# Kernel tuning notes

Measured on AMD Instinct MI355X. Metric: run time of the kernel, lower is better.

Reference implementation:

```python
import jax, jax.numpy as jnp
import numpy as np

B, N, C, H = 4, 2048, 1024, 16
HD = C // H  # head_dim = 64


def setup_inputs() -> dict:
    key = jax.random.key(0)
    ks = jax.random.split(key, 16)
    s = 0.02
    return {
        "x": jax.random.normal(ks[0], (B, N, C), dtype=jnp.float32),
        # qkv_proj: Linear(C, 3C): weight (3C, C), bias (3C,)
        "W_qkv": jax.random.normal(ks[1], (3 * C, C), dtype=jnp.float32) * s,
        "b_qkv": jax.random.normal(ks[2], (3 * C,), dtype=jnp.float32) * s,
        # out_proj: Linear(C, C)
        "W_out": jax.random.normal(ks[3], (C, C), dtype=jnp.float32) * s,
        "b_out": jax.random.normal(ks[4], (C,), dtype=jnp.float32) * s,
        # dynamically-reassigned position bias: shape (1, N, H, H) per the code's
        # (B, num_heads=N, seq_len=H, seq_len=H) score tensor
        "pos_bias": jax.random.normal(ks[5], (1, N, H, H), dtype=jnp.float32) * 0.01,
        # conv_proj: Linear(C, C)
        "W_cp": jax.random.normal(ks[6], (C, C), dtype=jnp.float32) * s,
        "b_cp": jax.random.normal(ks[7], (C,), dtype=jnp.float32) * s,
        # pointwise Conv1d(C, C, k=1): weight (C, C) after squeezing kernel dim
        "W_pw": jax.random.normal(ks[8], (C, C), dtype=jnp.float32) * s,
        "b_pw": jax.random.normal(ks[9], (C,), dtype=jnp.float32) * s,
        # depthwise Conv1d(C, C, k=3, groups=C): weight (C, 3)
        "W_dw": jax.random.normal(ks[10], (C, 3), dtype=jnp.float32) * s,
        "b_dw": jax.random.normal(ks[11], (C,), dtype=jnp.float32) * s,
        # token_wise_proj: Linear(C, C)
        "W_tw": jax.random.normal(ks[12], (C, C), dtype=jnp.float32) * s,
        "b_tw": jax.random.normal(ks[13], (C,), dtype=jnp.float32) * s,
    }


def reference(x, W_qkv, b_qkv, W_out, b_out, pos_bias, W_cp, b_cp,
              W_pw, b_pw, W_dw, b_dw, W_tw, b_tw) -> jnp.ndarray:
    Bx, Nx, Cx = x.shape
    scale = HD ** -0.5
    # qkv -> (B, N, H, 3*HD), chunk into q,k,v of (B, N, H, HD).
    # NOTE: faithful to the torch code, heads stay on axis 2; the matmul
    # contracts head_dim giving (B, N, H, H) scores (attention over heads).
    qkv = (x @ W_qkv.T + b_qkv).reshape(Bx, Nx, H, 3 * HD)
    q, k, v = jnp.split(qkv, 3, axis=-1)
    scores = jnp.einsum('bnhd,bngd->bnhg', q, k) * scale + pos_bias
    attn = jax.nn.softmax(scores, axis=-1)
    attn_out = jnp.einsum('bnhg,bngd->bnhd', attn, v).reshape(Bx, Nx, Cx)
    attn_out = attn_out @ W_out.T + b_out

    # Convolutional branch
    xc = x @ W_cp.T + b_cp          # conv_proj
    xc = xc @ W_pw.T + b_pw          # pointwise conv (k=1) == linear over channels
    xp = jnp.pad(xc, ((0, 0), (1, 1), (0, 0)))  # pad seq for k=3, padding=1
    xc = (xp[:, :-2] * W_dw[:, 0] + xp[:, 1:-1] * W_dw[:, 1]
          + xp[:, 2:] * W_dw[:, 2] + b_dw)      # depthwise conv
    xc = xc @ W_tw.T + b_tw          # token_wise_proj

    return attn_out + xc
```

## Files before the change

kernel.cpp:

```cpp
#include <hip/hip_runtime.h>
#include <hip/hip_bf16.h>
#include <stdint.h>

typedef __bf16 bf16_t;
typedef __attribute__((ext_vector_type(8))) __bf16 bf16x8;
typedef __attribute__((ext_vector_type(4))) __bf16 bf16x4;
typedef __attribute__((ext_vector_type(4))) float floatx4;
typedef __attribute__((ext_vector_type(4))) _Float16 half4_t;

#define GLDS16(g, l)                                                          \
  __builtin_amdgcn_global_load_lds(                                           \
      (const __attribute__((address_space(1))) void*)(g),                     \
      (__attribute__((address_space(3))) void*)(l), 16, 0, 0)

#define BAR8                                                                  \
  do {                                                                        \
    __builtin_amdgcn_s_barrier();                                             \
    __builtin_amdgcn_sched_barrier(0);                                        \
  } while (0)
#define VMCNT(n) asm volatile("s_waitcnt vmcnt(" #n ")")

template <int IT, int JT, typename OT>
__global__ __launch_bounds__(256) void gemm_bt(
    const bf16_t* __restrict__ A, const bf16_t* __restrict__ B,
    const float* __restrict__ bias, OT* __restrict__ C, int M, int N, int K) {
  constexpr int AROWS = 32 * IT;
  constexpr int BROWS = 32 * JT;
  constexpr int COLS = BROWS;
  constexpr int STAGE = (AROWS + BROWS) * 64;
  constexpr int EPI = (sizeof(OT) == 2) ? AROWS * COLS : 0;
  constexpr int SME = STAGE > EPI ? STAGE : EPI;
  __shared__ bf16_t sm[SME];
  bf16_t* As = sm;
  bf16_t* Bs = sm + AROWS * 64;

  const int tid = threadIdx.x;
  const int wave = tid >> 6;
  const int lane = tid & 63;
  const int quad = lane >> 4;
  const int l16 = lane & 15;
  const int m0 = blockIdx.x * AROWS;
  const int n0 = blockIdx.y * BROWS;
  const int wm = (wave >> 1) * (IT * 16);
  const int wn = (wave & 1) * (JT * 16);

  const int ra = wave * (8 * IT) + (lane >> 3);
  const int ga = ((lane & 7) ^ (ra & 7)) * 8;
  const int rb = wave * (8 * JT) + (lane >> 3);
  const int gb = ((lane & 7) ^ (rb & 7)) * 8;
  const bf16_t* Ab = A + (size_t)(m0 + ra) * K + ga;
  const bf16_t* Bb = B + (size_t)(n0 + rb) * K + gb;
  const int p0 = (quad ^ (l16 & 7)) * 8;

  floatx4 acc[IT][JT];
  const floatx4 zf = {0.f, 0.f, 0.f, 0.f};
#pragma unroll
  for (int i = 0; i < IT; ++i)
#pragma unroll
    for (int j = 0; j < JT; ++j) acc[i][j] = zf;

  for (int k0 = 0; k0 < K; k0 += 64) {
#pragma unroll
    for (int t = 0; t < IT; ++t)
      GLDS16(Ab + (size_t)(t * 8) * K + k0, As + (wave * (64 * IT) + t * 64) * 8);
#pragma unroll
    for (int t = 0; t < JT; ++t)
      GLDS16(Bb + (size_t)(t * 8) * K + k0, Bs + (wave * (64 * JT) + t * 64) * 8);
    __syncthreads();
#pragma unroll
    for (int ks = 0; ks < 2; ++ks) {
      const int ko = p0 ^ (ks * 32);
      bf16x8 af[IT], bfr[JT];
#pragma unroll
      for (int i = 0; i < IT; ++i)
        af[i] = *(const bf16x8*)(As + (wm + i * 16 + l16) * 64 + ko);
#pragma unroll
      for (int j = 0; j < JT; ++j)
        bfr[j] = *(const bf16x8*)(Bs + (wn + j * 16 + l16) * 64 + ko);
#pragma unroll
      for (int i = 0; i < IT; ++i)
#pragma unroll
        for (int j = 0; j < JT; ++j)
          acc[i][j] = __builtin_amdgcn_mfma_f32_16x16x32_bf16(
              bfr[j], af[i], acc[i][j], 0, 0, 0);
    }
    __syncthreads();
  }

  if constexpr (sizeof(OT) == 4) {
#pragma unroll
    for (int j = 0; j < JT; ++j) {
      const int colb = n0 + wn + j * 16 + quad * 4;
      floatx4 bv = zf;
      if (bias) bv = *(const floatx4*)(bias + colb);
#pragma unroll
      for (int i = 0; i < IT; ++i) {
        const int row = m0 + wm + i * 16 + l16;
        floatx4 v = acc[i][j] + bv;
        *(floatx4*)((float*)C + (size_t)row * N + colb) = v;
      }
    }
  } else {
    constexpr int SWZ = COLS / 32;
    constexpr int CPR = COLS / 8;
    constexpr int PASSES = (AROWS * CPR) / 256;
#pragma unroll
    for (int j = 0; j < JT; ++j) {
      const int colb = n0 + wn + j * 16 + quad * 4;
      floatx4 bv = zf;
      if (bias) bv = *(const floatx4*)(bias + colb);
      const int gcol = (wn + j * 16 + quad * 4) >> 2;
#pragma unroll
      for (int i = 0; i < IT; ++i) {
        const int rl = wm + i * 16 + l16;
        floatx4 v = acc[i][j] + bv;
        union {
          bf16_t b[4];
          uint2 u2;
        } pk;
        pk.b[0] = (bf16_t)v[0];
        pk.b[1] = (bf16_t)v[1];
        pk.b[2] = (bf16_t)v[2];
        pk.b[3] = (bf16_t)v[3];
        const int gsw = gcol ^ ((rl & 7) * SWZ);
        *(uint2*)(sm + rl * COLS + gsw * 4) = pk.u2;
      }
    }
    __syncthreads();
    bf16_t* Cb = (bf16_t*)C;
#pragma unroll
    for (int pass = 0; pass < PASSES; ++pass) {
      const int f = pass * 256 + tid;
      const int row = f / CPR;
      const int c16 = f % CPR;
      const int g0 = (2 * c16) ^ ((row & 7) * SWZ);
      uint4 v = *(const uint4*)(sm + row * COLS + g0 * 4);
      *(uint4*)(Cb + (size_t)(m0 + row) * N + n0 + c16 * 8) = v;
    }
  }
}

__global__ __launch_bounds__(512, 2) void gemm8p(
    const bf16_t* __restrict__ A, const bf16_t* __restrict__ B,
    const float* __restrict__ bias, bf16_t* __restrict__ C, int M, int N,
    int K) {
  __shared__ bf16_t sm8[65536];
  bf16_t* As = sm8;
  bf16_t* Bs = sm8 + 32768;

  const int tid = threadIdx.x;
  const int wave = tid >> 6, lane = tid & 63;
  const int l16 = lane & 15, quad = lane >> 4;
  const int wm = (wave >> 2) * 128, wn = (wave & 3) * 64;

  const int lin = blockIdx.y * gridDim.x + blockIdx.x;
  const int nwg = gridDim.x * gridDim.y;
  const int chunk = nwg >> 3;
  const int swz = (lin & 7) * chunk + (lin >> 3);
  const int bm = swz / gridDim.x;
  const int bn = swz % gridDim.x;
  const int m0 = bm << 8, n0 = bn << 8;

  const int srow = wave * 32 + (lane >> 2);
  const int kswz = ((lane & 3) * 8) ^ ((lane >> 5) << 4);
  const bf16_t* Ag = A + (size_t)(m0 + srow) * K + kswz;
  const bf16_t* Bg = B + (size_t)(n0 + srow) * K + kswz;
  const int sdst = wave * 1024;
  const size_t a16k = (size_t)K << 4;

  const int koe = (quad * 8) ^ ((l16 & 8) << 1);
  const int aoff = (wm + l16) * 32 + koe;
  const int boff = (wn + l16) * 32 + koe;

  floatx4 acc[8][4];
  const floatx4 zf = {0.f, 0.f, 0.f, 0.f};
#pragma unroll
  for (int i = 0; i < 8; ++i)
#pragma unroll
    for (int j = 0; j < 4; ++j) acc[i][j] = zf;

  bf16x8 af[4], bfr[4];

#define STG_A(buf, kh, TOFF)                                     \
  do {                                                           \
    bf16_t* _d = As + (buf)*16384 + (kh)*8192 + sdst;            \
    GLDS16(Ag + (TOFF) + (kh)*32, _d);                           \
    GLDS16(Ag + a16k + (TOFF) + (kh)*32, _d + 512);              \
  } while (0)
#define STG_B(buf, kh, TOFF)                                     \
  do {                                                           \
    bf16_t* _d = Bs + (buf)*16384 + (kh)*8192 + sdst;            \
    GLDS16(Bg + (TOFF) + (kh)*32, _d);                           \
    GLDS16(Bg + a16k + (TOFF) + (kh)*32, _d + 512);              \
  } while (0)
#define LDA4(buf, ks, mb)                                        \
  do {                                                           \
    const bf16_t* _p = As + (buf)*16384 + (ks)*8192 + aoff + (mb)*512; \
    af[0] = *(const bf16x8*)(_p);                                \
    af[1] = *(const bf16x8*)(_p + 512);                          \
    af[2] = *(const bf16x8*)(_p + 1024);                         \
    af[3] = *(const bf16x8*)(_p + 1536);                         \
  } while (0)
#define LDB4(buf, ks)                                            \
  do {                                                           \
    const bf16_t* _p = Bs + (buf)*16384 + (ks)*8192 + boff;      \
    bfr[0] = *(const bf16x8*)(_p);                               \
    bfr[1] = *(const bf16x8*)(_p + 512);                         \
    bfr[2] = *(const bf16x8*)(_p + 1024);                        \
    bfr[3] = *(const bf16x8*)(_p + 1536);                        \
  } while (0)
#define MFMA16(mb)                                               \
  do {                                                           \
    __builtin_amdgcn_s_setprio(1);                               \
    _Pragma("unroll") for (int _i = 0; _i < 4; ++_i)             \
        _Pragma("unroll") for (int _j = 0; _j < 4; ++_j)         \
            acc[(mb) + _i][_j] =                                 \
                __builtin_amdgcn_mfma_f32_16x16x32_bf16(         \
                    bfr[_j], af[_i], acc[(mb) + _i][_j], 0, 0, 0); \
    __builtin_amdgcn_s_setprio(0);                               \
  } while (0)

  STG_A(0, 0, 0);
  STG_A(0, 1, 0);
  STG_B(0, 0, 0);
  STG_B(0, 1, 0);
  STG_B(1, 0, 64);
  STG_A(1, 0, 64);
  STG_B(1, 1, 64);
  VMCNT(6);
  BAR8;

  const int NT = K >> 6;
  for (int it = 0; it < NT / 2 - 1; ++it) {
    LDA4(0, 0, 0); LDB4(0, 0); STG_A(1, 1, 64);            BAR8; MFMA16(0); BAR8;
    LDA4(0, 0, 4);             STG_B(0, 0, 128);           BAR8; MFMA16(4); BAR8;
    LDA4(0, 1, 0); LDB4(0, 1); STG_A(0, 0, 128);           BAR8; MFMA16(0); BAR8;
    LDA4(0, 1, 4);             STG_B(0, 1, 128); VMCNT(6); BAR8; MFMA16(4); BAR8;
    LDA4(1, 0, 0); LDB4(1, 0); STG_A(0, 1, 128);           BAR8; MFMA16(0); BAR8;
    LDA4(1, 0, 4);             STG_B(1, 0, 192);           BAR8; MFMA16(4); BAR8;
    LDA4(1, 1, 0); LDB4(1, 1); STG_A(1, 0, 192);           BAR8; MFMA16(0); BAR8;
    LDA4(1, 1, 4);             STG_B(1, 1, 192); VMCNT(6); BAR8; MFMA16(4); BAR8;
    Ag += 128;
    Bg += 128;
  }
  LDA4(0, 0, 0); LDB4(0, 0); STG_A(1, 1, 64); BAR8; MFMA16(0); BAR8;
  LDA4(0, 0, 4);                              BAR8; MFMA16(4); BAR8;
  LDA4(0, 1, 0); LDB4(0, 1);                  BAR8; MFMA16(0); BAR8;
  LDA4(0, 1, 4);             VMCNT(0);        BAR8; MFMA16(4); BAR8;
  LDA4(1, 0, 0); LDB4(1, 0);                  BAR8; MFMA16(0); BAR8;
  LDA4(1, 0, 4);                              BAR8; MFMA16(4); BAR8;
  LDA4(1, 1, 0); LDB4(1, 1);                  BAR8; MFMA16(0); BAR8;
  LDA4(1, 1, 4);                              BAR8; MFMA16(4); BAR8;

  const int crow_b = wm + l16;
#pragma unroll
  for (int nj = 0; nj < 4; ++nj) {
    const int colb = wn + nj * 16 + quad * 4;
    floatx4 bv = zf;
    if (bias) bv = *(const floatx4*)(bias + n0 + colb);
#pragma unroll
    for (int mi = 0; mi < 8; ++mi) {
      const int row = crow_b + mi * 16;
      floatx4 v = acc[mi][nj] + bv;
      union {
        bf16_t b[4];
        uint2 u2;
      } pk;
      pk.b[0] = (bf16_t)v[0];
      pk.b[1] = (bf16_t)v[1];
      pk.b[2] = (bf16_t)v[2];
      pk.b[3] = (bf16_t)v[3];
      const int cb = (colb * 2) ^ ((row & 31) << 4);
      *(uint2*)((char*)sm8 + row * 512 + cb) = pk.u2;
    }
  }
  __syncthreads();
#pragma unroll
  for (int pass = 0; pass < 16; ++pass) {
    const int flat = pass * 8192 + tid * 16;
    const int row = flat >> 9;
    const int cb = flat & 511;
    const int cbs = cb ^ ((row & 31) << 4);
    uint4 v = *(const uint4*)((char*)sm8 + row * 512 + cbs);
    *(uint4*)((char*)C + ((size_t)(m0 + row) * N + n0) * 2 + cb) = v;
  }
#undef STG_A
#undef STG_B
#undef LDA4
#undef LDB4
#undef MFMA16
}

__global__ __launch_bounds__(512, 2) void gemm8p2(
    const bf16_t* __restrict__ A, const bf16_t* __restrict__ B,
    const float* __restrict__ bias, float* __restrict__ C, int M, int N,
    int K) {
  __shared__ bf16_t sm2[49152];
  bf16_t* As = sm2;
  bf16_t* Bs = sm2 + 16384;

  const int tid = threadIdx.x;
  const int wave = tid >> 6, lane = tid & 63;
  const int l16 = lane & 15, quad = lane >> 4;
  const int wm = (wave >> 2) * 64, wn = (wave & 3) * 64;
  const int m0 = blockIdx.y << 7, n0 = blockIdx.x << 8;

  const int srA = wave * 16 + (lane >> 2);
  const int srB = wave * 32 + (lane >> 2);
  const int kswz = ((lane & 3) * 8) ^ ((lane >> 5) << 4);
  const bf16_t* Ag = A + (size_t)(m0 + srA) * K + kswz;
  const bf16_t* Bg = B + (size_t)(n0 + srB) * K + kswz;
  const size_t b16k = (size_t)K << 4;

  const int koe = (quad * 8) ^ ((l16 & 8) << 1);
  const int aoff = (wm + l16) * 32 + koe;
  const int boff = (wn + l16) * 32 + koe;

  floatx4 acc[4][4];
  const floatx4 zf = {0.f, 0.f, 0.f, 0.f};
#pragma unroll
  for (int i = 0; i < 4; ++i)
#pragma unroll
    for (int j = 0; j < 4; ++j) acc[i][j] = zf;

  bf16x8 af[4], bfr[4];

#define SA2(buf, kh, TOFF)                                                 \
  GLDS16(Ag + (TOFF) + (kh)*32, As + (buf)*8192 + (kh)*4096 + wave * 512)
#define SB2(buf, kh, TOFF)                                                 \
  do {                                                                     \
    bf16_t* _d = Bs + (buf)*16384 + (kh)*8192 + wave * 1024;               \
    GLDS16(Bg + (TOFF) + (kh)*32, _d);                                     \
    GLDS16(Bg + b16k + (TOFF) + (kh)*32, _d + 512);                        \
  } while (0)
#define LD2(buf, kh)                                                       \
  do {                                                                     \
    const bf16_t* _pa = As + (buf)*8192 + (kh)*4096 + aoff;                \
    const bf16_t* _pb = Bs + (buf)*16384 + (kh)*8192 + boff;               \
    _Pragma("unroll") for (int _i = 0; _i < 4; ++_i)                       \
        af[_i] = *(const bf16x8*)(_pa + _i * 512);                         \
    _Pragma("unroll") for (int _j = 0; _j < 4; ++_j)                       \
        bfr[_j] = *(const bf16x8*)(_pb + _j * 512);                        \
  } while (0)
#define MM2                                                                \
  do {                                                                     \
    __builtin_amdgcn_s_setprio(1);                                         \
    _Pragma("unroll") for (int _i = 0; _i < 4; ++_i)                       \
        _Pragma("unroll") for (int _j = 0; _j < 4; ++_j)                   \
            acc[_i][_j] = __builtin_amdgcn_mfma_f32_16x16x32_bf16(         \
                bfr[_j], af[_i], acc[_i][_j], 0, 0, 0);                    \
    __builtin_amdgcn_s_setprio(0);                                         \
  } while (0)

  SA2(0, 0, 0);
  SB2(0, 0, 0);
  SA2(0, 1, 0);
  SB2(0, 1, 0);
  SA2(1, 0, 64);
  SB2(1, 0, 64);
  VMCNT(3);
  BAR8;

  const int NT = K >> 6;
  for (int it = 0; it < NT / 2 - 1; ++it) {
    LD2(0, 0); SA2(1, 1, 64);  SB2(1, 1, 64);            BAR8; MM2; BAR8;
    LD2(0, 1); SA2(0, 0, 128); SB2(0, 0, 128); VMCNT(3); BAR8; MM2; BAR8;
    LD2(1, 0); SA2(0, 1, 128); SB2(0, 1, 128);           BAR8; MM2; BAR8;
    LD2(1, 1); SA2(1, 0, 192); SB2(1, 0, 192); VMCNT(3); BAR8; MM2; BAR8;
    Ag += 128;
    Bg += 128;
  }
  LD2(0, 0); SA2(1, 1, 64); SB2(1, 1, 64); BAR8; MM2; BAR8;
  LD2(0, 1); VMCNT(0);                     BAR8; MM2; BAR8;
  LD2(1, 0);                               BAR8; MM2; BAR8;
  LD2(1, 1);                                     MM2;

#pragma unroll
  for (int j = 0; j < 4; ++j) {
    const int colb = n0 + wn + j * 16 + quad * 4;
    floatx4 bv = zf;
    if (bias) bv = *(const floatx4*)(bias + colb);
#pragma unroll
    for (int i = 0; i < 4; ++i) {
      const int row = m0 + wm + i * 16 + l16;
      floatx4 v = acc[i][j] + bv;
      *(floatx4*)(C + (size_t)row * N + colb) = v;
    }
  }
#undef SA2
#undef SB2
#undef LD2
#undef MM2
}

__global__ __launch_bounds__(256) void prep2_k(
    const float* __restrict__ x, bf16_t* __restrict__ x_bf,
    const float* __restrict__ Wqkv, bf16_t* __restrict__ Wbig1,
    const float* __restrict__ Wpw, bf16_t* __restrict__ Wpw_bf,
    const float* __restrict__ Wout, const float* __restrict__ Wtw,
    bf16_t* __restrict__ Wbig2, const float* __restrict__ bqkv,
    float* __restrict__ bias1, const float* __restrict__ bout,
    const float* __restrict__ btw, float* __restrict__ bias2,
    const float* __restrict__ Wcp, bf16_t* __restrict__ WcpT,
    const float* __restrict__ bcp, const float* __restrict__ bpw) {
  __shared__ float t[32][33];
  const int b = blockIdx.x, tid = threadIdx.x;
  auto cvt4 = [](const float* in, bf16_t* out, int i) {
    floatx4 v = ((const floatx4*)in)[i];
    bf16x4 o;
    o[0] = (bf16_t)v[0];
    o[1] = (bf16_t)v[1];
    o[2] = (bf16_t)v[2];
    o[3] = (bf16_t)v[3];
    ((bf16x4*)out)[i] = o;
  };
  if (b < 8192) {
    cvt4(x, x_bf, b * 256 + tid);
  } else if (b < 11264) {
    cvt4(Wqkv, Wbig1, (b - 8192) * 256 + tid);
  } else if (b < 12288) {
    cvt4(Wpw, Wpw_bf, (b - 11264) * 256 + tid);
  } else if (b < 14336) {
    const bool second = b >= 13312;
    int i = (b - (second ? 13312 : 12288)) * 256 + tid;
    floatx4 v = ((const floatx4*)(second ? Wtw : Wout))[i];
    bf16x4 o;
    o[0] = (bf16_t)v[0];
    o[1] = (bf16_t)v[1];
    o[2] = (bf16_t)v[2];
    o[3] = (bf16_t)v[3];
    int row = i >> 8, c4 = i & 255;
    *(bf16x4*)(Wbig2 + (size_t)row * 2048 + (second ? 1024 : 0) + c4 * 4) = o;
  } else if (b < 14339) {
    int i = (b - 14336) * 256 + tid;
    if (i < 768) ((floatx4*)bias1)[i] = ((const floatx4*)bqkv)[i];
  } else if (b == 14339) {
    ((floatx4*)bias2)[tid] =
        ((const floatx4*)bout)[tid] + ((const floatx4*)btw)[tid];
  } else if (b < 15364) {
    const int tb = b - 14340;
    const int bx = (tb & 31) * 32, by = (tb >> 5) * 32;
    const int tx = tid & 31, ty = tid >> 5;
#pragma unroll
    for (int iq = 0; iq < 4; ++iq)
      t[ty + iq * 8][tx] = Wcp[(size_t)(by + ty + iq * 8) * 1024 + bx + tx];
    __syncthreads();
#pragma unroll
    for (int iq = 0; iq < 4; ++iq)
      WcpT[(size_t)(bx + ty + iq * 8) * 1024 + by + tx] =
          (bf16_t)t[tx][ty + iq * 8];
  } else {
    const int row = (b - 15364) * 4 + (tid >> 6);
    const int l = tid & 63;
    const float* wr = Wpw + (size_t)row * 1024;
    float s = 0.f;
    for (int j = l; j < 1024; j += 64) s += wr[j] * bcp[j];
#pragma unroll
    for (int o = 32; o > 0; o >>= 1) s += __shfl_down(s, o);
    if (l == 0) bias1[3072 + row] = s + bpw[row];
  }
}

static __device__ inline void exp8(uint32_t w0, uint32_t w1, uint32_t w2,
                                   uint32_t w3, float* f) {
  f[0] = __uint_as_float(w0 << 16);
  f[1] = __uint_as_float(w0 & 0xffff0000u);
  f[2] = __uint_as_float(w1 << 16);
  f[3] = __uint_as_float(w1 & 0xffff0000u);
  f[4] = __uint_as_float(w2 << 16);
  f[5] = __uint_as_float(w2 & 0xffff0000u);
  f[6] = __uint_as_float(w3 << 16);
  f[7] = __uint_as_float(w3 & 0xffff0000u);
}

__global__ __launch_bounds__(256) void mid_k(const bf16_t* __restrict__ G1,
                                             const float* __restrict__ pos,
                                             const float* __restrict__ Wdw,
                                             const float* __restrict__ bdw,
                                             bf16_t* __restrict__ Mid) {
  __shared__ bf16_t ost[4][16 * 68];
  const int tid = threadIdx.x;
  if (blockIdx.x < 2048) {
    const int wave = tid >> 6, lane = tid & 63;
    const int p = blockIdx.x * 4 + wave;
    const int l16 = lane & 15, quad = lane >> 4;
    const bf16_t* row = G1 + (size_t)p * 4096;
    const bf16_t* qb = row + l16 * 192 + quad * 8;

    bf16x8 q0 = *(const bf16x8*)(qb);
    bf16x8 q1 = *(const bf16x8*)(qb + 32);
    bf16x8 k0 = *(const bf16x8*)(qb + 64);
    bf16x8 k1 = *(const bf16x8*)(qb + 96);
    floatx4 S = {0.f, 0.f, 0.f, 0.f};
    S = __builtin_amdgcn_mfma_f32_16x16x32_bf16(k0, q0, S, 0, 0, 0);
    S = __builtin_amdgcn_mfma_f32_16x16x32_bf16(k1, q1, S, 0, 0, 0);

    const floatx4 pb = *(const floatx4*)(pos + (size_t)(p & 2047) * 256 +
                                         l16 * 16 + quad * 4);
    float v[4];
#pragma unroll
    for (int r = 0; r < 4; ++r) v[r] = S[r] * 0.125f + pb[r];

    float m = fmaxf(fmaxf(v[0], v[1]), fmaxf(v[2], v[3]));
    m = fmaxf(m, __shfl_xor(m, 16));
    m = fmaxf(m, __shfl_xor(m, 32));
    float e[4], sum = 0.f;
#pragma unroll
    for (int r = 0; r < 4; ++r) {
      e[r] = __expf(v[r] - m);
      sum += e[r];
    }
    sum += __shfl_xor(sum, 16);
    sum += __shfl_xor(sum, 32);
    const float inv = 1.0f / sum;
    half4_t pa;
#pragma unroll
    for (int r = 0; r < 4; ++r) pa[r] = (_Float16)(e[r] * inv);

    const bf16_t* vb_base = row + 128 + l16;
    const floatx4 zf = {0.f, 0.f, 0.f, 0.f};
    floatx4 o[4];
#pragma unroll
    for (int t = 0; t < 4; ++t) {
      half4_t vb;
#pragma unroll
      for (int j = 0; j < 4; ++j)
        vb[j] = (_Float16)(float)vb_base[(quad * 4 + j) * 192 + t * 16];
      o[t] = __builtin_amdgcn_mfma_f32_16x16x16f16(pa, vb, zf, 0, 0, 0);
    }

    bf16_t* ow = ost[wave];
#pragma unroll
    for (int r = 0; r < 4; ++r)
#pragma unroll
      for (int t = 0; t < 4; ++t)
        ow[(quad * 4 + r) * 68 + t * 16 + l16] = (bf16_t)o[t][r];
    const int h2 = lane >> 2, m4 = lane & 3;
    const bf16_t* srcp = ow + h2 * 68 + m4 * 16;
    uint2 a0 = *(const uint2*)(srcp);
    uint2 a1 = *(const uint2*)(srcp + 4);
    uint2 a2 = *(const uint2*)(srcp + 8);
    uint2 a3 = *(const uint2*)(srcp + 12);
    uint4 s0 = {a0.x, a0.y, a1.x, a1.y};
    uint4 s1 = {a2.x, a2.y, a3.x, a3.y};
    uint4* dst = (uint4*)(Mid + (size_t)p * 2048 + h2 * 64 + m4 * 16);
    dst[0] = s0;
    dst[1] = s1;
  } else {
    const bf16_t* in = G1 + 3072;
    bf16_t* out = Mid + 1024;
    const int item = (blockIdx.x - 2048) * 256 + tid;
    const int cc = item & 127, rowg = item >> 7;
    const int c0 = cc * 8;
    float w0[8], w1[8], w2[8], bb[8];
#pragma unroll
    for (int c = 0; c < 8; ++c) {
      w0[c] = Wdw[(c0 + c) * 3];
      w1[c] = Wdw[(c0 + c) * 3 + 1];
      w2[c] = Wdw[(c0 + c) * 3 + 2];
      bb[c] = bdw[c0 + c];
    }
#pragma unroll
    for (int jr = 0; jr < 4; ++jr) {
      const int tt = rowg * 4 + jr;
      const int n = tt & 2047;
      const bf16_t* ip = in + (size_t)tt * 4096 + c0;
      const uint4 z4 = {0, 0, 0, 0};
      uint4 um = (n > 0) ? *(const uint4*)(ip - 4096) : z4;
      uint4 uc = *(const uint4*)(ip);
      uint4 up = (n < 2047) ? *(const uint4*)(ip + 4096) : z4;
      float fm[8], fc[8], fp[8];
      exp8(um.x, um.y, um.z, um.w, fm);
      exp8(uc.x, uc.y, uc.z, uc.w, fc);
      exp8(up.x, up.y, up.z, up.w, fp);
      union {
        bf16_t b[8];
        uint4 u;
      } pk;
#pragma unroll
      for (int c = 0; c < 8; ++c)
        pk.b[c] =
            (bf16_t)(bb[c] + fm[c] * w0[c] + fc[c] * w1[c] + fp[c] * w2[c]);
      *(uint4*)(out + (size_t)tt * 2048 + c0) = pk.u;
    }
  }
}

extern "C" void kernel_launch(void* const* d_in, const int* in_sizes, int n_in,
                              void* d_out, int out_size, void* d_ws,
                              size_t ws_size, hipStream_t stream) {
  (void)in_sizes; (void)n_in; (void)out_size; (void)ws_size;
  const float* x = (const float*)d_in[0];
  const float* Wqkv = (const float*)d_in[1];
  const float* bqkv = (const float*)d_in[2];
  const float* Wout = (const float*)d_in[3];
  const float* bout = (const float*)d_in[4];
  const float* pos = (const float*)d_in[5];
  const float* Wcp = (const float*)d_in[6];
  const float* bcp = (const float*)d_in[7];
  const float* Wpw = (const float*)d_in[8];
  const float* bpw = (const float*)d_in[9];
  const float* Wdw = (const float*)d_in[10];
  const float* bdw = (const float*)d_in[11];
  const float* Wtw = (const float*)d_in[12];
  const float* btw = (const float*)d_in[13];
  float* out = (float*)d_out;

  char* ws = (char*)d_ws;
  const size_t MB = 1024ull * 1024ull;
  bf16_t* x_bf = (bf16_t*)(ws + 0);
  bf16_t* Wbig1 = (bf16_t*)(ws + 16 * MB);
  bf16_t* WcpT = (bf16_t*)(ws + 24 * MB);
  bf16_t* Wpw_bf = (bf16_t*)(ws + 26 * MB);
  bf16_t* Mid = (bf16_t*)(ws + 0);
  bf16_t* Wbig2 = (bf16_t*)(ws + 32 * MB);
  float* bias1 = (float*)(ws + 36 * MB);
  float* bias2 = (float*)(ws + 36 * MB + 65536);
  bf16_t* G1out = (bf16_t*)(ws + 37 * MB);

  prep2_k<<<15620, 256, 0, stream>>>(x, x_bf, Wqkv, Wbig1, Wpw, Wpw_bf, Wout,
                                     Wtw, Wbig2, bqkv, bias1, bout, btw, bias2,
                                     Wcp, WcpT, bcp, bpw);

  gemm_bt<2, 2, bf16_t><<<dim3(16, 16), 256, 0, stream>>>(
      Wpw_bf, WcpT, nullptr, Wbig1 + (size_t)3072 * 1024, 1024, 1024, 1024);

  gemm8p<<<dim3(16, 32), 512, 0, stream>>>(x_bf, Wbig1, bias1, G1out, 8192,
                                           4096, 1024);

  mid_k<<<3072, 256, 0, stream>>>(G1out, pos, Wdw, bdw, Mid);

  gemm8p2<<<dim3(4, 64), 512, 0, stream>>>(Mid, Wbig2, bias2, out, 8192, 1024,
                                           2048);
}
```

Before: 275.7 us.

## Double-buffer LDS fragment registers to prefetch next MFMA operands early

Both GEMM kernels now keep two sets of A/B fragment registers and load the next sub-tile from LDS one stage ahead of the MFMA block that consumes the current set, so LDS read latency overlaps matrix math. The global-to-LDS staging waits (vmcnt) are reshuffled to match the new ordering, the MFMA loop order is swapped to iterate j outermost, and an explicit sync is added before the epilogue. The extra fragment registers raise VGPR pressure, which may hurt occupancy, and the retuned wait counts must still guarantee LDS data is ready before it is read.

```diff
diff --git a/kernel.cpp b/kernel.cpp
--- a/kernel.cpp
+++ b/kernel.cpp
@@ -179,7 +179,7 @@
 #pragma unroll
     for (int j = 0; j < 4; ++j) acc[i][j] = zf;
 
-  bf16x8 af[4], bfr[4];
+  bf16x8 afA[4], afB[4], bfr[4];
 
 #define STG_A(buf, kh, TOFF)                                     \
   do {                                                           \
@@ -192,14 +192,6 @@
     bf16_t* _d = Bs + (buf)*16384 + (kh)*8192 + sdst;            \
     GLDS16(Bg + (TOFF) + (kh)*32, _d);                           \
     GLDS16(Bg + a16k + (TOFF) + (kh)*32, _d + 512);              \
-  } while (0)
-#define LDA4(buf, ks, mb)                                        \
-  do {                                                           \
-    const bf16_t* _p = As + (buf)*16384 + (ks)*8192 + aoff + (mb)*512; \
-    af[0] = *(const bf16x8*)(_p);                                \
-    af[1] = *(const bf16x8*)(_p + 512);                          \
-    af[2] = *(const bf16x8*)(_p + 1024);                         \
-    af[3] = *(const bf16x8*)(_p + 1536);                         \
   } while (0)
 #define LDB4(buf, ks)                                            \
   do {                                                           \
@@ -209,14 +201,23 @@
     bfr[2] = *(const bf16x8*)(_p + 1024);                        \
     bfr[3] = *(const bf16x8*)(_p + 1536);                        \
   } while (0)
-#define MFMA16(mb)                                               \
+#define LDA4(buf, ks, mb, DST)                                   \
+  do {                                                           \
+    const bf16_t* _p =                                           \
+        As + (buf)*16384 + (ks)*8192 + aoff + (mb)*512;          \
+    DST[0] = *(const bf16x8*)(_p);                               \
+    DST[1] = *(const bf16x8*)(_p + 512);                         \
+    DST[2] = *(const bf16x8*)(_p + 1024);                        \
+    DST[3] = *(const bf16x8*)(_p + 1536);                        \
+  } while (0)
+#define MFMA16(AF, mb)                                           \
   do {                                                           \
     __builtin_amdgcn_s_setprio(1);                               \
-    _Pragma("unroll") for (int _i = 0; _i < 4; ++_i)             \
-        _Pragma("unroll") for (int _j = 0; _j < 4; ++_j)         \
+    _Pragma("unroll") for (int _j = 0; _j < 4; ++_j)             \
+        _Pragma("unroll") for (int _i = 0; _i < 4; ++_i)         \
             acc[(mb) + _i][_j] =                                 \
                 __builtin_amdgcn_mfma_f32_16x16x32_bf16(         \
-                    bfr[_j], af[_i], acc[(mb) + _i][_j], 0, 0, 0); \
+                    bfr[_j], AF[_i], acc[(mb) + _i][_j], 0, 0, 0); \
     __builtin_amdgcn_s_setprio(0);                               \
   } while (0)
 
@@ -229,28 +230,30 @@
   STG_B(1, 1, 64);
   VMCNT(6);
   BAR8;
+  LDA4(0, 0, 0, afA);
 
   const int NT = K >> 6;
   for (int it = 0; it < NT / 2 - 1; ++it) {
-    LDA4(0, 0, 0); LDB4(0, 0); STG_A(1, 1, 64);            BAR8; MFMA16(0); BAR8;
-    LDA4(0, 0, 4);             STG_B(0, 0, 128);           BAR8; MFMA16(4); BAR8;
-    LDA4(0, 1, 0); LDB4(0, 1); STG_A(0, 0, 128);           BAR8; MFMA16(0); BAR8;
-    LDA4(0, 1, 4);             STG_B(0, 1, 128); VMCNT(6); BAR8; MFMA16(4); BAR8;
-    LDA4(1, 0, 0); LDB4(1, 0); STG_A(0, 1, 128);           BAR8; MFMA16(0); BAR8;
-    LDA4(1, 0, 4);             STG_B(1, 0, 192);           BAR8; MFMA16(4); BAR8;
-    LDA4(1, 1, 0); LDB4(1, 1); STG_A(1, 0, 192);           BAR8; MFMA16(0); BAR8;
-    LDA4(1, 1, 4);             STG_B(1, 1, 192); VMCNT(6); BAR8; MFMA16(4); BAR8;
+    LDB4(0, 0); LDA4(0, 0, 4, afB); STG_A(1, 1, 64);  VMCNT(8); BAR8; MFMA16(afA, 0); BAR8;
+    LDA4(0, 1, 0, afA);             STG_B(0, 0, 128);           BAR8; MFMA16(afB, 4); BAR8;
+    LDB4(0, 1); LDA4(0, 1, 4, afB); STG_A(0, 0, 128); VMCNT(8); BAR8; MFMA16(afA, 0); BAR8;
+    LDA4(1, 0, 0, afA);             STG_B(0, 1, 128);           BAR8; MFMA16(afB, 4); BAR8;
+    LDB4(1, 0); LDA4(1, 0, 4, afB); STG_A(0, 1, 128); VMCNT(8); BAR8; MFMA16(afA, 0); BAR8;
+    LDA4(1, 1, 0, afA);             STG_B(1, 0, 192);           BAR8; MFMA16(afB, 4); BAR8;
+    LDB4(1, 1); LDA4(1, 1, 4, afB); STG_A(1, 0, 192); VMCNT(8); BAR8; MFMA16(afA, 0); BAR8;
+    LDA4(0, 0, 0, afA);             STG_B(1, 1, 192);           BAR8; MFMA16(afB, 4); BAR8;
     Ag += 128;
     Bg += 128;
   }
-  LDA4(0, 0, 0); LDB4(0, 0); STG_A(1, 1, 64); BAR8; MFMA16(0); BAR8;
-  LDA4(0, 0, 4);                              BAR8; MFMA16(4); BAR8;
-  LDA4(0, 1, 0); LDB4(0, 1);                  BAR8; MFMA16(0); BAR8;
-  LDA4(0, 1, 4);             VMCNT(0);        BAR8; MFMA16(4); BAR8;
-  LDA4(1, 0, 0); LDB4(1, 0);                  BAR8; MFMA16(0); BAR8;
-  LDA4(1, 0, 4);                              BAR8; MFMA16(4); BAR8;
-  LDA4(1, 1, 0); LDB4(1, 1);                  BAR8; MFMA16(0); BAR8;
-  LDA4(1, 1, 4);                              BAR8; MFMA16(4); BAR8;
+  LDB4(0, 0); LDA4(0, 0, 4, afB); STG_A(1, 1, 64); VMCNT(8); BAR8; MFMA16(afA, 0); BAR8;
+  LDA4(0, 1, 0, afA);                                         BAR8; MFMA16(afB, 4); BAR8;
+  LDB4(0, 1); LDA4(0, 1, 4, afB);                  VMCNT(4); BAR8; MFMA16(afA, 0); BAR8;
+  LDA4(1, 0, 0, afA);                                         BAR8; MFMA16(afB, 4); BAR8;
+  LDB4(1, 0); LDA4(1, 0, 4, afB);                  VMCNT(0); BAR8; MFMA16(afA, 0); BAR8;
+  LDA4(1, 1, 0, afA);                                         BAR8; MFMA16(afB, 4); BAR8;
+  LDB4(1, 1); LDA4(1, 1, 4, afB);                             BAR8; MFMA16(afA, 0); BAR8;
+  MFMA16(afB, 4);
+  __syncthreads();
 
   const int crow_b = wm + l16;
 #pragma unroll
@@ -286,8 +289,8 @@
   }
 #undef STG_A
 #undef STG_B
+#undef LDB4
 #undef LDA4
-#undef LDB4
 #undef MFMA16
 }
 
@@ -323,7 +326,7 @@
 #pragma unroll
     for (int j = 0; j < 4; ++j) acc[i][j] = zf;
 
-  bf16x8 af[4], bfr[4];
+  bf16x8 afA[4], afB[4], bfA[4], bfB[4];
 
 #define SA2(buf, kh, TOFF)                                                 \
   GLDS16(Ag + (TOFF) + (kh)*32, As + (buf)*8192 + (kh)*4096 + wave * 512)
@@ -333,22 +336,22 @@
     GLDS16(Bg + (TOFF) + (kh)*32, _d);                                     \
     GLDS16(Bg + b16k + (TOFF) + (kh)*32, _d + 512);                        \
   } while (0)
-#define LD2(buf, kh)                                                       \
+#define LD2(buf, kh, AF, BF)                                               \
   do {                                                                     \
     const bf16_t* _pa = As + (buf)*8192 + (kh)*4096 + aoff;                \
     const bf16_t* _pb = Bs + (buf)*16384 + (kh)*8192 + boff;               \
     _Pragma("unroll") for (int _i = 0; _i < 4; ++_i)                       \
-        af[_i] = *(const bf16x8*)(_pa + _i * 512);                         \
+        AF[_i] = *(const bf16x8*)(_pa + _i * 512);                         \
     _Pragma("unroll") for (int _j = 0; _j < 4; ++_j)                       \
-        bfr[_j] = *(const bf16x8*)(_pb + _j * 512);                        \
-  } while (0)
-#define MM2                                                                \
+        BF[_j] = *(const bf16x8*)(_pb + _j * 512);                         \
+  } while (0)
+#define MM2(AF, BF)                                                        \
   do {                                                                     \
     __builtin_amdgcn_s_setprio(1);                                         \
-    _Pragma("unroll") for (int _i = 0; _i < 4; ++_i)                       \
-        _Pragma("unroll") for (int _j = 0; _j < 4; ++_j)                   \
+    _Pragma("unroll") for (int _j = 0; _j < 4; ++_j)                       \
+        _Pragma("unroll") for (int _i = 0; _i < 4; ++_i)                   \
             acc[_i][_j] = __builtin_amdgcn_mfma_f32_16x16x32_bf16(         \
-                bfr[_j], af[_i], acc[_i][_j], 0, 0, 0);                    \
+                BF[_j], AF[_i], acc[_i][_j], 0, 0, 0);                     \
     __builtin_amdgcn_s_setprio(0);                                         \
   } while (0)
 
@@ -360,20 +363,21 @@
   SB2(1, 0, 64);
   VMCNT(3);
   BAR8;
+  LD2(0, 0, afA, bfA);
 
   const int NT = K >> 6;
   for (int it = 0; it < NT / 2 - 1; ++it) {
-    LD2(0, 0); SA2(1, 1, 64);  SB2(1, 1, 64);            BAR8; MM2; BAR8;
-    LD2(0, 1); SA2(0, 0, 128); SB2(0, 0, 128); VMCNT(3); BAR8; MM2; BAR8;
-    LD2(1, 0); SA2(0, 1, 128); SB2(0, 1, 128);           BAR8; MM2; BAR8;
-    LD2(1, 1); SA2(1, 0, 192); SB2(1, 0, 192); VMCNT(3); BAR8; MM2; BAR8;
+    LD2(0, 1, afB, bfB); SA2(1, 1, 64);  SB2(1, 1, 64);  VMCNT(3); BAR8; MM2(afA, bfA); BAR8;
+    LD2(1, 0, afA, bfA); SA2(0, 0, 128); SB2(0, 0, 128); VMCNT(3); BAR8; MM2(afB, bfB); BAR8;
+    LD2(1, 1, afB, bfB); SA2(0, 1, 128); SB2(0, 1, 128); VMCNT(3); BAR8; MM2(afA, bfA); BAR8;
+    LD2(0, 0, afA, bfA); SA2(1, 0, 192); SB2(1, 0, 192); VMCNT(3); BAR8; MM2(afB, bfB); BAR8;
     Ag += 128;
     Bg += 128;
   }
-  LD2(0, 0); SA2(1, 1, 64); SB2(1, 1, 64); BAR8; MM2; BAR8;
-  LD2(0, 1); VMCNT(0);                     BAR8; MM2; BAR8;
-  LD2(1, 0);                               BAR8; MM2; BAR8;
-  LD2(1, 1);                                     MM2;
+  LD2(0, 1, afB, bfB); SA2(1, 1, 64); SB2(1, 1, 64); VMCNT(3); BAR8; MM2(afA, bfA); BAR8;
+  LD2(1, 0, afA, bfA); VMCNT(0);                               BAR8; MM2(afB, bfB); BAR8;
+  LD2(1, 1, afB, bfB);                                         BAR8; MM2(afA, bfA); BAR8;
+  MM2(afB, bfB);
 
 #pragma unroll
   for (int j = 0; j < 4; ++j) {
```

Result: no change. 273.7 us (-0.7%).
